# Kernel optimization log

Measured on AMD Instinct MI355X. Metric: run time of the kernel, lower is better.

## Reference

```python
import jax, jax.numpy as jnp
import numpy as np

B, C, H, W = 4, 256, 64, 64
EPS = 1e-6


def setup_inputs() -> dict:
    key = jax.random.key(0)
    ks = jax.random.split(key, 6)
    x = jax.random.normal(ks[0], (B, C, H, W), jnp.float32)
    gn_w = jnp.ones((1, C, 1, 1), jnp.float32)
    gn_b = jnp.zeros((1, C, 1, 1), jnp.float32)
    s = 1.0 / np.sqrt(C)
    w0 = jax.random.normal(ks[1], (C, C), jnp.float32) * s
    w1 = jax.random.normal(ks[2], (C, C), jnp.float32) * s
    w2 = jax.random.normal(ks[3], (C, C), jnp.float32) * s
    w3 = jax.random.normal(ks[4], (C, C), jnp.float32) * s
    b0 = jnp.zeros((C,), jnp.float32)
    b1 = jnp.zeros((C,), jnp.float32)
    b2 = jnp.zeros((C,), jnp.float32)
    b3 = jnp.zeros((C,), jnp.float32)
    return {"x": x, "gn_w": gn_w, "gn_b": gn_b,
            "w0": w0, "b0": b0, "w1": w1, "b1": b1,
            "w2": w2, "b2": b2, "w3": w3, "b3": b3}


def _nin(t, Wm, bv):
    # 1x1 conv as channel matmul: (B,C,H,W) x (C,D) -> (B,D,H,W)
    return jnp.einsum('bchw,cd->bdhw', t, Wm) + bv[None, :, None, None]


def reference(x, gn_w, gn_b, w0, b0, w1, b1, w2, b2, w3, b3):
    Bb, Cc, Hh, Ww = x.shape
    G = min(Cc // 4, 32)  # GroupLayerNorm2d groups
    # per-pixel group norm: normalize over channels within each group only
    xg = x.reshape(Bb, G, Cc // G, Hh, Ww)
    mean = xg.mean(axis=2, keepdims=True)
    var = xg.var(axis=2, keepdims=True)
    hn = ((xg - mean) / jnp.sqrt(var + EPS)).reshape(Bb, Cc, Hh, Ww)
    hn = hn * gn_w + gn_b
    q = _nin(hn, w0, b0)
    k = _nin(hn, w1, b1)
    v = _nin(hn, w2, b2)
    # full (B,H,W,H,W) scores; mask is causal along W only (key col j > query col w)
    scores = jnp.einsum('bchw,bcij->bhwij', q, k) * (float(Cc) ** -0.5)
    causal = jnp.triu(jnp.ones((Ww, Ww), bool), k=1)  # (W_query, W_key)
    scores = jnp.where(causal[None, None, :, None, :], -jnp.inf, scores)
    attn = jax.nn.softmax(scores.reshape(Bb, Hh, Ww, Hh * Ww), axis=-1)
    attn = attn.reshape(Bb, Hh, Ww, Hh, Ww)
    h = jnp.einsum('bhwij,bcij->bchw', attn, v)
    return x + _nin(h, w3, b3)  # skip_rescale=False
```

## Files before the change

### kernel.cpp

```cpp
#include <hip/hip_runtime.h>
#include <math.h>

#define LOG2E 1.4426950408889634f

typedef __attribute__((ext_vector_type(8))) __bf16 bf16x8_t;
typedef __attribute__((ext_vector_type(8))) short short8_t;
typedef __attribute__((ext_vector_type(4))) short short4_t;
typedef __attribute__((ext_vector_type(4))) float f32x4;

static __device__ __forceinline__ short f2bf(float f){
    unsigned u = __builtin_bit_cast(unsigned, f);
    unsigned r = (u + 0x7fffu + ((u >> 16) & 1u)) >> 16;
    return (short)r;
}
static __device__ __forceinline__ float bf2f(short s){
    return __builtin_bit_cast(float, (unsigned)((unsigned short)s) << 16);
}

static __device__ __forceinline__ f32x4 mfma16(short8_t a, short8_t b, f32x4 c){
    return __builtin_amdgcn_mfma_f32_16x16x32_bf16(
        __builtin_bit_cast(bf16x8_t, a), __builtin_bit_cast(bf16x8_t, b), c, 0, 0, 0);
}

static __device__ __forceinline__ float swz16(float v){
    return __builtin_bit_cast(float,
        __builtin_amdgcn_ds_swizzle(__builtin_bit_cast(int, v), 0x401F));
}
static __device__ __forceinline__ float bperm32(int addr, float v){
    return __builtin_bit_cast(float,
        __builtin_amdgcn_ds_bpermute(addr, __builtin_bit_cast(int, v)));
}

__global__ __launch_bounds__(256) void prep_w(const float* __restrict__ w0,
    const float* __restrict__ w1, const float* __restrict__ w2,
    const float* __restrict__ w3, short* __restrict__ wT)
{
    __shared__ float T[64 * 65];
    const int mat = blockIdx.x >> 4, tile = blockIdx.x & 15;
    const int c0 = (tile >> 2) * 64, d0 = (tile & 3) * 64;
    const float* src = mat == 0 ? w0 : mat == 1 ? w1 : mat == 2 ? w2 : w3;
    const int t = threadIdx.x;
    #pragma unroll
    for (int i = 0; i < 4; i++){
        int r = (t >> 4) + i * 16, c4 = (t & 15) * 4;
        f32x4 v = *(const f32x4*)(src + (size_t)(c0 + r) * 256 + d0 + c4);
        #pragma unroll
        for (int j = 0; j < 4; j++) T[r * 65 + c4 + j] = v[j];
    }
    __syncthreads();
    int drow = t >> 2, cb = (t & 3) * 16;
    short tmp[16];
    #pragma unroll
    for (int j = 0; j < 16; j++) tmp[j] = f2bf(T[(cb + j) * 65 + drow]);
    short* dst = wT + (size_t)mat * 65536 + (size_t)(d0 + drow) * 256 + c0 + cb;
    *(short8_t*)dst = *(short8_t*)tmp;
    *(short8_t*)(dst + 8) = *(short8_t*)(tmp + 8);
}

__global__ __launch_bounds__(256) void gn_kernel(const float* __restrict__ x,
    const float* __restrict__ gnw, const float* __restrict__ gnb,
    short* __restrict__ hn)
{
    int flat = blockIdx.x * 256 + threadIdx.x;
    int n = flat & 4095, g = (flat >> 12) & 31, b = flat >> 17;
    const float* xp = x + (size_t)(b * 256 + g * 8) * 4096 + n;
    float v[8], s = 0.f, s2 = 0.f;
    #pragma unroll
    for (int k = 0; k < 8; k++){ float t = xp[(size_t)k * 4096]; v[k] = t; s += t; s2 += t * t; }
    float mean = s * 0.125f;
    float var  = s2 * 0.125f - mean * mean;
    float inv  = rsqrtf(var + 1e-6f);
    int h = n >> 6, w = n & 63, m = w * 64 + h;
    short o[8];
    #pragma unroll
    for (int k = 0; k < 8; k++)
        o[k] = f2bf((v[k] - mean) * inv * gnw[g * 8 + k] + gnb[g * 8 + k]);
    *(short8_t*)(hn + (size_t)(b * 4096 + m) * 256 + g * 8) = *(short8_t*)o;
}

__global__ __launch_bounds__(256) void qkv_gemm(const short* __restrict__ hn,
    const short* __restrict__ wT, const float* __restrict__ bq,
    const float* __restrict__ bk, const float* __restrict__ bv,
    short* __restrict__ Q, short* __restrict__ Kf, short* __restrict__ Vf)
{
    __shared__ short As[64 * 72];
    __shared__ short Bs[64 * 72];
    __shared__ float CT[64 * 65];

    const int tid = threadIdx.x;
    const int m0 = blockIdx.x * 64;
    const int by = blockIdx.y;
    const int mat = by >> 2;
    const int d0 = (by & 3) * 64;
    const short* w = wT + mat * 65536;
    const float* bias = mat == 0 ? bq : mat == 1 ? bk : bv;

    const int wv = tid >> 6, lane = tid & 63;
    const int wrow = (wv >> 1) * 32, wcol = (wv & 1) * 32;
    const int lrow = lane & 15, lq = lane >> 4;

    f32x4 acc[2][2] = {};

    for (int k0 = 0; k0 < 256; k0 += 64){
        __syncthreads();
        #pragma unroll
        for (int i = 0; i < 2; i++){
            int idx = tid + i * 256, r = idx >> 3, c = (idx & 7) * 8;
            *(short8_t*)&As[r * 72 + c] = *(const short8_t*)(hn + (size_t)(m0 + r) * 256 + k0 + c);
            *(short8_t*)&Bs[r * 72 + c] = *(const short8_t*)(w  + (size_t)(d0 + r) * 256 + k0 + c);
        }
        __syncthreads();
        #pragma unroll
        for (int kk = 0; kk < 2; kk++){
            int off = kk * 32 + lq * 8;
            short8_t a0  = *(short8_t*)&As[(wrow + lrow) * 72 + off];
            short8_t a1  = *(short8_t*)&As[(wrow + 16 + lrow) * 72 + off];
            short8_t b0v = *(short8_t*)&Bs[(wcol + lrow) * 72 + off];
            short8_t b1v = *(short8_t*)&Bs[(wcol + 16 + lrow) * 72 + off];
            acc[0][0] = mfma16(a0, b0v, acc[0][0]);
            acc[0][1] = mfma16(a0, b1v, acc[0][1]);
            acc[1][0] = mfma16(a1, b0v, acc[1][0]);
            acc[1][1] = mfma16(a1, b1v, acc[1][1]);
        }
    }

    const int b = m0 >> 12, kb64 = (m0 & 4095) >> 6;

    if (mat == 0){
        #pragma unroll
        for (int i = 0; i < 2; i++)
          #pragma unroll
          for (int j = 0; j < 2; j++)
            #pragma unroll
            for (int r = 0; r < 4; r++){
                int row = wrow + i * 16 + lq * 4 + r;
                int col = wcol + j * 16 + lrow;
                Q[(size_t)(m0 + row) * 256 + d0 + col] = f2bf((acc[i][j][r] + bias[d0 + col]) * 0.0625f);
            }
    } else if (mat == 1){
        #pragma unroll
        for (int i = 0; i < 2; i++)
          #pragma unroll
          for (int j = 0; j < 2; j++)
            #pragma unroll
            for (int r = 0; r < 4; r++){
                int row = wrow + i * 16 + lq * 4 + r;
                int col = wcol + j * 16 + lrow;
                CT[row * 65 + col] = acc[i][j][r] + bias[d0 + col];
            }
        __syncthreads();
        int key = tid >> 2, c16 = (tid & 3) * 16;
        int kc = key >> 4, l15 = key & 15;
        #pragma unroll
        for (int half = 0; half < 2; half++){
            int ch0 = c16 + half * 8;
            int ks = (d0 + ch0) >> 5, lqf = (ch0 & 31) >> 3;
            short tmp[8];
            #pragma unroll
            for (int j = 0; j < 8; j++) tmp[j] = f2bf(CT[key * 65 + ch0 + j]);
            size_t base = ((((size_t)(b * 64 + kb64)) * 4 + kc) * 8 + ks) * 512 + (lqf * 16 + l15) * 8;
            *(short8_t*)(Kf + base) = *(short8_t*)tmp;
        }
    } else {
        #pragma unroll
        for (int i = 0; i < 2; i++)
          #pragma unroll
          for (int j = 0; j < 2; j++)
            #pragma unroll
            for (int r = 0; r < 4; r++){
                int row = wrow + i * 16 + lq * 4 + r;
                int col = wcol + j * 16 + lrow;
                CT[col * 65 + row] = acc[i][j][r] + bias[d0 + col];
            }
        __syncthreads();
        const int kbd = kb64 >> 1, parity = kb64 & 1;
        const int cht_l = tid >> 6, lane_s = tid & 63;
        const int l15s = lane_s & 15, lg4s = lane_s >> 4;
        const int cht = (d0 >> 4) + cht_l;
        #pragma unroll
        for (int kc = 0; kc < 4; kc++){
            short tmp[4];
            #pragma unroll
            for (int j = 0; j < 4; j++)
                tmp[j] = f2bf(CT[(cht_l * 16 + l15s) * 65 + kc * 16 + lg4s * 4 + j]);
            size_t base = (size_t)b * 1048576 + (size_t)kbd * 32768 + kc * 8192
                        + cht * 512 + lane_s * 8 + parity * 4;
            *(short4_t*)(Vf + base) = *(short4_t*)tmp;
        }
    }
}

static __device__ __forceinline__ void sm_update(const f32x4& st, float& m, float& l,
    f32x4* __restrict__ oacc, f32x4* __restrict__ pa, f32x4& p, int a32)
{
    float tmax = fmaxf(fmaxf(st[0], st[1]), fmaxf(st[2], st[3]));
    tmax = fmaxf(tmax, swz16(tmax));
    tmax = fmaxf(tmax, bperm32(a32, tmax));
    if (!__all(tmax <= m + 5.0f)){
        float mn = fmaxf(m, tmax);
        float alpha = exp2f((m - mn) * LOG2E);
        l *= alpha;
        #pragma unroll
        for (int i = 0; i < 16; i++){
            f32x4 t = oacc[i];
            #pragma unroll
            for (int r = 0; r < 4; r++) t[r] *= alpha;
            oacc[i] = t;
        }
        if (pa){
            #pragma unroll
            for (int r = 0; r < 4; r++) (*pa)[r] *= alpha;
        }
        m = mn;
    }
    #pragma unroll
    for (int r = 0; r < 4; r++) p[r] = exp2f((st[r] - m) * LOG2E);
    float ts = (p[0] + p[1]) + (p[2] + p[3]);
    ts += swz16(ts);
    ts += bperm32(a32, ts);
    l += ts;
}

__global__ __launch_bounds__(256, 2) void attn_kernel(const short* __restrict__ Q,
    const short* __restrict__ Kf, const short* __restrict__ Vf,
    short* __restrict__ hb)
{
    __shared__ float mls[4][32][2];
    __shared__ short LOs[4][32][264];

    const int tid = threadIdx.x, lane = tid & 63, kc = tid >> 6;
    const int l15 = lane & 15, lg4 = lane >> 4;
    const int a32 = ((lane ^ 32) << 2);

    const int id  = blockIdx.x;
    const int xcd = id & 7;
    const int b   = xcd >> 1;
    const int hh  = xcd & 1;
    const int r_  = id >> 3;
    const int t_  = r_ & 31;
    const int w   = (r_ >> 5) ? 63 - t_ : t_;
    const int q0  = w * 64 + hh * 32;

    const short* Kb = Kf + (size_t)b * 1048576 + kc * 4096 + lane * 8;
    const short* Vb = Vf + (size_t)b * 1048576 + kc * 8192 + lane * 8;

    short8_t qf0[8], qf1[8];
    {
        const short* qp0 = Q + ((size_t)b * 4096 + q0 + l15) * 256;
        const short* qp1 = qp0 + 16 * 256;
        #pragma unroll
        for (int ks = 0; ks < 8; ks++){
            qf0[ks] = *(const short8_t*)(qp0 + ks * 32 + lg4 * 8);
            qf1[ks] = *(const short8_t*)(qp1 + ks * 32 + lg4 * 8);
        }
    }

    f32x4 oacc0[16] = {}, oacc1[16] = {};
    float m0 = -1e30f, l0 = 0.f;
    float m1 = -1e30f, l1 = 0.f;

    for (int kb = 0; kb <= w; kb += 2){
        short8_t kf[8];
        {
            const short* ka = Kb + (size_t)kb * 16384;
            #pragma unroll
            for (int ks = 0; ks < 8; ks++) kf[ks] = *(const short8_t*)(ka + ks * 512);
        }
        f32x4 stA0 = {}, stA1 = {};
        #pragma unroll
        for (int ks = 0; ks < 8; ks++){
            stA0 = mfma16(kf[ks], qf0[ks], stA0);
            stA1 = mfma16(kf[ks], qf1[ks], stA1);
        }
        f32x4 pa0, pa1;
        sm_update(stA0, m0, l0, oacc0, nullptr, pa0, a32);
        sm_update(stA1, m1, l1, oacc1, nullptr, pa1, a32);

        f32x4 pb0 = {0.f, 0.f, 0.f, 0.f}, pb1 = {0.f, 0.f, 0.f, 0.f};
        if (kb + 1 <= w){
            const short* ka = Kb + (size_t)(kb + 1) * 16384;
            #pragma unroll
            for (int ks = 0; ks < 8; ks++) kf[ks] = *(const short8_t*)(ka + ks * 512);
            f32x4 stB0 = {}, stB1 = {};
            #pragma unroll
            for (int ks = 0; ks < 8; ks++){
                stB0 = mfma16(kf[ks], qf0[ks], stB0);
                stB1 = mfma16(kf[ks], qf1[ks], stB1);
            }
            sm_update(stB0, m0, l0, oacc0, &pa0, pb0, a32);
            sm_update(stB1, m1, l1, oacc1, &pa1, pb1, a32);
        }

        short pk0[8], pk1[8];
        #pragma unroll
        for (int r = 0; r < 4; r++){
            pk0[r] = f2bf(pa0[r]); pk0[4 + r] = f2bf(pb0[r]);
            pk1[r] = f2bf(pa1[r]); pk1[4 + r] = f2bf(pb1[r]);
        }
        short8_t pbf0 = *(short8_t*)pk0;
        short8_t pbf1 = *(short8_t*)pk1;

        const short* vit = Vb + (size_t)(kb >> 1) * 32768;
        #pragma unroll
        for (int cht = 0; cht < 16; cht++){
            short8_t vfr = *(const short8_t*)(vit + cht * 512);
            oacc0[cht] = mfma16(vfr, pbf0, oacc0[cht]);
            oacc1[cht] = mfma16(vfr, pbf1, oacc1[cht]);
        }
    }

    if (lg4 == 0){
        mls[kc][l15][0] = m0;      mls[kc][l15][1] = l0;
        mls[kc][16 + l15][0] = m1; mls[kc][16 + l15][1] = l1;
    }
    __syncthreads();
    float sc0, sc1;
    {
        float ms0 = fmaxf(fmaxf(mls[0][l15][0], mls[1][l15][0]),
                          fmaxf(mls[2][l15][0], mls[3][l15][0]));
        float ms1 = fmaxf(fmaxf(mls[0][16 + l15][0], mls[1][16 + l15][0]),
                          fmaxf(mls[2][16 + l15][0], mls[3][16 + l15][0]));
        sc0 = exp2f((m0 - ms0) * LOG2E);
        sc1 = exp2f((m1 - ms1) * LOG2E);
    }
    #pragma unroll
    for (int cht = 0; cht < 16; cht++){
        short t4[4];
        #pragma unroll
        for (int r = 0; r < 4; r++) t4[r] = f2bf(oacc0[cht][r] * sc0);
        *(short4_t*)&LOs[kc][l15][cht * 16 + lg4 * 4] = *(short4_t*)t4;
        #pragma unroll
        for (int r = 0; r < 4; r++) t4[r] = f2bf(oacc1[cht][r] * sc1);
        *(short4_t*)&LOs[kc][16 + l15][cht * 16 + lg4 * 4] = *(short4_t*)t4;
    }
    __syncthreads();
    {
        const int qq = tid & 31, cc = tid >> 5;
        float mv0 = mls[0][qq][0], mv1 = mls[1][qq][0], mv2 = mls[2][qq][0], mv3 = mls[3][qq][0];
        float ms = fmaxf(fmaxf(mv0, mv1), fmaxf(mv2, mv3));
        float Ls = mls[0][qq][1] * exp2f((mv0 - ms) * LOG2E)
                 + mls[1][qq][1] * exp2f((mv1 - ms) * LOG2E)
                 + mls[2][qq][1] * exp2f((mv2 - ms) * LOG2E)
                 + mls[3][qq][1] * exp2f((mv3 - ms) * LOG2E);
        float inv = 1.f / Ls;
        const int h = hh * 32 + qq;
        short* dst = hb + ((size_t)b * 4096 + h * 64 + w) * 256 + cc * 32;
        #pragma unroll
        for (int c8 = 0; c8 < 4; c8++){
            short8_t a0 = *(const short8_t*)&LOs[0][qq][cc * 32 + c8 * 8];
            short8_t a1 = *(const short8_t*)&LOs[1][qq][cc * 32 + c8 * 8];
            short8_t a2 = *(const short8_t*)&LOs[2][qq][cc * 32 + c8 * 8];
            short8_t a3 = *(const short8_t*)&LOs[3][qq][cc * 32 + c8 * 8];
            short t8[8];
            #pragma unroll
            for (int j = 0; j < 8; j++){
                float s = (bf2f(a0[j]) + bf2f(a1[j])) + (bf2f(a2[j]) + bf2f(a3[j]));
                t8[j] = f2bf(s * inv);
            }
            *(short8_t*)(dst + c8 * 8) = *(short8_t*)t8;
        }
    }
}

__global__ __launch_bounds__(256) void final_gemm(const short* __restrict__ hbuf,
    const short* __restrict__ wT3, const float* __restrict__ b3,
    const float* __restrict__ x, float* __restrict__ out)
{
    __shared__ short As[64 * 72];
    __shared__ short Bs[64 * 72];
    __shared__ float CT[64 * 65];

    const int tid = threadIdx.x;
    const int m0 = blockIdx.x * 64;
    const int d0 = blockIdx.y * 64;
    const int wv = tid >> 6, lane = tid & 63;
    const int wrow = (wv >> 1) * 32, wcol = (wv & 1) * 32;
    const int lrow = lane & 15, lq = lane >> 4;

    f32x4 acc[2][2] = {};
    for (int k0 = 0; k0 < 256; k0 += 64){
        __syncthreads();
        #pragma unroll
        for (int i = 0; i < 2; i++){
            int idx = tid + i * 256, r = idx >> 3, c = (idx & 7) * 8;
            *(short8_t*)&As[r * 72 + c] = *(const short8_t*)(hbuf + (size_t)(m0 + r) * 256 + k0 + c);
            *(short8_t*)&Bs[r * 72 + c] = *(const short8_t*)(wT3 + (size_t)(d0 + r) * 256 + k0 + c);
        }
        __syncthreads();
        #pragma unroll
        for (int kk = 0; kk < 2; kk++){
            int off = kk * 32 + lq * 8;
            short8_t a0  = *(short8_t*)&As[(wrow + lrow) * 72 + off];
            short8_t a1  = *(short8_t*)&As[(wrow + 16 + lrow) * 72 + off];
            short8_t b0v = *(short8_t*)&Bs[(wcol + lrow) * 72 + off];
            short8_t b1v = *(short8_t*)&Bs[(wcol + 16 + lrow) * 72 + off];
            acc[0][0] = mfma16(a0, b0v, acc[0][0]);
            acc[0][1] = mfma16(a0, b1v, acc[0][1]);
            acc[1][0] = mfma16(a1, b0v, acc[1][0]);
            acc[1][1] = mfma16(a1, b1v, acc[1][1]);
        }
    }
    #pragma unroll
    for (int i = 0; i < 2; i++)
      #pragma unroll
      for (int j = 0; j < 2; j++)
        #pragma unroll
        for (int r = 0; r < 4; r++){
            int row = wrow + i * 16 + lq * 4 + r;
            int col = wcol + j * 16 + lrow;
            CT[col * 65 + row] = acc[i][j][r] + b3[d0 + col];
        }
    __syncthreads();
    int b = m0 >> 12, n0 = m0 & 4095, hrow = n0 >> 6;
    int dr = tid >> 2, wc = (tid & 3) * 16;
    size_t base = ((size_t)(b * 256 + d0 + dr) * 64 + hrow) * 64 + wc;
    const f32x4* xp = (const f32x4*)(x + base);
    f32x4* op = (f32x4*)(out + base);
    #pragma unroll
    for (int q = 0; q < 4; q++){
        f32x4 xv = xp[q], o;
        #pragma unroll
        for (int j = 0; j < 4; j++) o[j] = xv[j] + CT[dr * 65 + wc + q * 4 + j];
        op[q] = o;
    }
}

extern "C" void kernel_launch(void* const* d_in, const int* in_sizes, int n_in,
                              void* d_out, int out_size, void* d_ws, size_t ws_size,
                              hipStream_t stream)
{
    const float* x   = (const float*)d_in[0];
    const float* gnw = (const float*)d_in[1];
    const float* gnb = (const float*)d_in[2];
    const float* w0  = (const float*)d_in[3];
    const float* b0  = (const float*)d_in[4];
    const float* w1  = (const float*)d_in[5];
    const float* b1  = (const float*)d_in[6];
    const float* w2  = (const float*)d_in[7];
    const float* b2  = (const float*)d_in[8];
    const float* w3  = (const float*)d_in[9];
    const float* b3  = (const float*)d_in[10];
    float* out = (float*)d_out;

    char* ws = (char*)d_ws;
    short* wT  = (short*)(ws);
    short* hn  = (short*)(ws + 524288);
    short* Qb  = (short*)(ws + 8912896);
    short* Kfb = (short*)(ws + 17301504);
    short* Vfb = (short*)(ws + 25690112);
    short* hb  = (short*)(ws + 34078720);

    prep_w   <<<64, 256, 0, stream>>>(w0, w1, w2, w3, wT);
    gn_kernel<<<2048, 256, 0, stream>>>(x, gnw, gnb, hn);
    qkv_gemm <<<dim3(256, 12), 256, 0, stream>>>(hn, wT, b0, b1, b2, Qb, Kfb, Vfb);
    attn_kernel<<<512, 256, 0, stream>>>(Qb, Kfb, Vfb, hb);
    final_gemm<<<dim3(256, 4), 256, 0, stream>>>(hb, wT + 3 * 65536, b3, x, out);
}
```

Baseline: 244.3 us.

## Prefetch K fragments and stage V via async global-to-LDS loads in attention

```diff
diff --git a/kernel.cpp b/kernel.cpp
--- a/kernel.cpp
+++ b/kernel.cpp
@@ -29,6 +29,12 @@
 static __device__ __forceinline__ float bperm32(int addr, float v){
     return __builtin_bit_cast(float,
         __builtin_amdgcn_ds_bpermute(addr, __builtin_bit_cast(int, v)));
+}
+
+static __device__ __forceinline__ void gload_lds16(const void* g, void* l){
+    __builtin_amdgcn_global_load_lds(
+        (const __attribute__((address_space(1))) unsigned char*)g,
+        (__attribute__((address_space(3))) unsigned char*)l, 16, 0, 0);
 }
 
 __global__ __launch_bounds__(256) void prep_w(const float* __restrict__ w0,
@@ -190,43 +196,12 @@
     }
 }
 
-static __device__ __forceinline__ void sm_update(const f32x4& st, float& m, float& l,
-    f32x4* __restrict__ oacc, f32x4* __restrict__ pa, f32x4& p, int a32)
-{
-    float tmax = fmaxf(fmaxf(st[0], st[1]), fmaxf(st[2], st[3]));
-    tmax = fmaxf(tmax, swz16(tmax));
-    tmax = fmaxf(tmax, bperm32(a32, tmax));
-    if (!__all(tmax <= m + 5.0f)){
-        float mn = fmaxf(m, tmax);
-        float alpha = exp2f((m - mn) * LOG2E);
-        l *= alpha;
-        #pragma unroll
-        for (int i = 0; i < 16; i++){
-            f32x4 t = oacc[i];
-            #pragma unroll
-            for (int r = 0; r < 4; r++) t[r] *= alpha;
-            oacc[i] = t;
-        }
-        if (pa){
-            #pragma unroll
-            for (int r = 0; r < 4; r++) (*pa)[r] *= alpha;
-        }
-        m = mn;
-    }
-    #pragma unroll
-    for (int r = 0; r < 4; r++) p[r] = exp2f((st[r] - m) * LOG2E);
-    float ts = (p[0] + p[1]) + (p[2] + p[3]);
-    ts += swz16(ts);
-    ts += bperm32(a32, ts);
-    l += ts;
-}
-
 __global__ __launch_bounds__(256, 2) void attn_kernel(const short* __restrict__ Q,
     const short* __restrict__ Kf, const short* __restrict__ Vf,
     short* __restrict__ hb)
 {
+    __shared__ short SH[4 * 32 * 264];
     __shared__ float mls[4][32][2];
-    __shared__ short LOs[4][32][264];
 
     const int tid = threadIdx.x, lane = tid & 63, kc = tid >> 6;
     const int l15 = lane & 15, lg4 = lane >> 4;
@@ -238,11 +213,12 @@
     const int hh  = xcd & 1;
     const int r_  = id >> 3;
     const int t_  = r_ & 31;
-    const int w   = (r_ >> 5) ? 63 - t_ : t_;
+    const int w   = (r_ & 32) ? 63 - t_ : t_;
     const int q0  = w * 64 + hh * 32;
 
     const short* Kb = Kf + (size_t)b * 1048576 + kc * 4096 + lane * 8;
-    const short* Vb = Vf + (size_t)b * 1048576 + kc * 8192 + lane * 8;
+    const short* Vg = Vf + (size_t)b * 1048576 + kc * 8192 + lane * 8;
+    short* Vl = &SH[kc * 8192];
 
     short8_t qf0[8], qf1[8];
     {
@@ -259,59 +235,124 @@
     float m0 = -1e30f, l0 = 0.f;
     float m1 = -1e30f, l1 = 0.f;
 
+    short8_t kf[8];
+    #pragma unroll
+    for (int ks = 0; ks < 8; ks++) kf[ks] = *(const short8_t*)(Kb + ks * 512);
+
     for (int kb = 0; kb <= w; kb += 2){
-        short8_t kf[8];
-        {
-            const short* ka = Kb + (size_t)kb * 16384;
-            #pragma unroll
-            for (int ks = 0; ks < 8; ks++) kf[ks] = *(const short8_t*)(ka + ks * 512);
-        }
+        const bool has_odd = (kb + 1 <= w);
+
         f32x4 stA0 = {}, stA1 = {};
         #pragma unroll
         for (int ks = 0; ks < 8; ks++){
             stA0 = mfma16(kf[ks], qf0[ks], stA0);
             stA1 = mfma16(kf[ks], qf1[ks], stA1);
         }
-        f32x4 pa0, pa1;
-        sm_update(stA0, m0, l0, oacc0, nullptr, pa0, a32);
-        sm_update(stA1, m1, l1, oacc1, nullptr, pa1, a32);
-
-        f32x4 pb0 = {0.f, 0.f, 0.f, 0.f}, pb1 = {0.f, 0.f, 0.f, 0.f};
-        if (kb + 1 <= w){
+        if (has_odd){
             const short* ka = Kb + (size_t)(kb + 1) * 16384;
             #pragma unroll
             for (int ks = 0; ks < 8; ks++) kf[ks] = *(const short8_t*)(ka + ks * 512);
+        }
+        {
+            const short* vsrc = Vg + (size_t)(kb >> 1) * 32768;
+            #pragma unroll
+            for (int i = 0; i < 16; i++)
+                gload_lds16(vsrc + i * 512, Vl + i * 512);
+        }
+
+        f32x4 pA0, pA1;
+        {
+            float tl0 = fmaxf(fmaxf(stA0[0], stA0[1]), fmaxf(stA0[2], stA0[3]));
+            float tl1 = fmaxf(fmaxf(stA1[0], stA1[1]), fmaxf(stA1[2], stA1[3]));
+            if (!__all(tl0 <= m0 + 5.f && tl1 <= m1 + 5.f)){
+                float tm0 = fmaxf(tl0, swz16(tl0)); tm0 = fmaxf(tm0, bperm32(a32, tm0));
+                float tm1 = fmaxf(tl1, swz16(tl1)); tm1 = fmaxf(tm1, bperm32(a32, tm1));
+                float mn0 = fmaxf(m0, tm0), mn1 = fmaxf(m1, tm1);
+                float al0 = exp2f((m0 - mn0) * LOG2E), al1 = exp2f((m1 - mn1) * LOG2E);
+                l0 *= al0; l1 *= al1;
+                #pragma unroll
+                for (int i = 0; i < 16; i++){
+                    #pragma unroll
+                    for (int r = 0; r < 4; r++){ oacc0[i][r] *= al0; oacc1[i][r] *= al1; }
+                }
+                m0 = mn0; m1 = mn1;
+            }
+            #pragma unroll
+            for (int r = 0; r < 4; r++){
+                pA0[r] = exp2f((stA0[r] - m0) * LOG2E);
+                pA1[r] = exp2f((stA1[r] - m1) * LOG2E);
+            }
+            l0 += (pA0[0] + pA0[1]) + (pA0[2] + pA0[3]);
+            l1 += (pA1[0] + pA1[1]) + (pA1[2] + pA1[3]);
+        }
+
+        f32x4 pB0 = {0.f, 0.f, 0.f, 0.f}, pB1 = {0.f, 0.f, 0.f, 0.f};
+        if (has_odd){
             f32x4 stB0 = {}, stB1 = {};
             #pragma unroll
             for (int ks = 0; ks < 8; ks++){
                 stB0 = mfma16(kf[ks], qf0[ks], stB0);
                 stB1 = mfma16(kf[ks], qf1[ks], stB1);
             }
-            sm_update(stB0, m0, l0, oacc0, &pa0, pb0, a32);
-            sm_update(stB1, m1, l1, oacc1, &pa1, pb1, a32);
+            if (kb + 2 <= w){
+                const short* ka = Kb + (size_t)(kb + 2) * 16384;
+                #pragma unroll
+                for (int ks = 0; ks < 8; ks++) kf[ks] = *(const short8_t*)(ka + ks * 512);
+            }
+            float tl0 = fmaxf(fmaxf(stB0[0], stB0[1]), fmaxf(stB0[2], stB0[3]));
+            float tl1 = fmaxf(fmaxf(stB1[0], stB1[1]), fmaxf(stB1[2], stB1[3]));
+            if (!__all(tl0 <= m0 + 5.f && tl1 <= m1 + 5.f)){
+                float tm0 = fmaxf(tl0, swz16(tl0)); tm0 = fmaxf(tm0, bperm32(a32, tm0));
+                float tm1 = fmaxf(tl1, swz16(tl1)); tm1 = fmaxf(tm1, bperm32(a32, tm1));
+                float mn0 = fmaxf(m0, tm0), mn1 = fmaxf(m1, tm1);
+                float al0 = exp2f((m0 - mn0) * LOG2E), al1 = exp2f((m1 - mn1) * LOG2E);
+                l0 *= al0; l1 *= al1;
+                #pragma unroll
+                for (int i = 0; i < 16; i++){
+                    #pragma unroll
+                    for (int r = 0; r < 4; r++){ oacc0[i][r] *= al0; oacc1[i][r] *= al1; }
+                }
+                #pragma unroll
+                for (int r = 0; r < 4; r++){ pA0[r] *= al0; pA1[r] *= al1; }
+                m0 = mn0; m1 = mn1;
+            }
+            #pragma unroll
+            for (int r = 0; r < 4; r++){
+                pB0[r] = exp2f((stB0[r] - m0) * LOG2E);
+                pB1[r] = exp2f((stB1[r] - m1) * LOG2E);
+            }
+            l0 += (pB0[0] + pB0[1]) + (pB0[2] + pB0[3]);
+            l1 += (pB1[0] + pB1[1]) + (pB1[2] + pB1[3]);
         }
 
         short pk0[8], pk1[8];
         #pragma unroll
         for (int r = 0; r < 4; r++){
-            pk0[r] = f2bf(pa0[r]); pk0[4 + r] = f2bf(pb0[r]);
-            pk1[r] = f2bf(pa1[r]); pk1[4 + r] = f2bf(pb1[r]);
+            pk0[r] = f2bf(pA0[r]); pk0[4 + r] = f2bf(pB0[r]);
+            pk1[r] = f2bf(pA1[r]); pk1[4 + r] = f2bf(pB1[r]);
         }
         short8_t pbf0 = *(short8_t*)pk0;
         short8_t pbf1 = *(short8_t*)pk1;
 
-        const short* vit = Vb + (size_t)(kb >> 1) * 32768;
+        if (kb + 2 <= w){
+            asm volatile("s_waitcnt vmcnt(8)" ::: "memory");
+        } else {
+            asm volatile("s_waitcnt vmcnt(0)" ::: "memory");
+        }
         #pragma unroll
         for (int cht = 0; cht < 16; cht++){
-            short8_t vfr = *(const short8_t*)(vit + cht * 512);
+            short8_t vfr = *(const short8_t*)(Vl + cht * 512 + lane * 8);
             oacc0[cht] = mfma16(vfr, pbf0, oacc0[cht]);
             oacc1[cht] = mfma16(vfr, pbf1, oacc1[cht]);
         }
     }
 
+    float l0t = l0 + swz16(l0); l0t += bperm32(a32, l0t);
+    float l1t = l1 + swz16(l1); l1t += bperm32(a32, l1t);
+
     if (lg4 == 0){
-        mls[kc][l15][0] = m0;      mls[kc][l15][1] = l0;
-        mls[kc][16 + l15][0] = m1; mls[kc][16 + l15][1] = l1;
+        mls[kc][l15][0] = m0;      mls[kc][l15][1] = l0t;
+        mls[kc][16 + l15][0] = m1; mls[kc][16 + l15][1] = l1t;
     }
     __syncthreads();
     float sc0, sc1;
@@ -328,10 +369,10 @@
         short t4[4];
         #pragma unroll
         for (int r = 0; r < 4; r++) t4[r] = f2bf(oacc0[cht][r] * sc0);
-        *(short4_t*)&LOs[kc][l15][cht * 16 + lg4 * 4] = *(short4_t*)t4;
+        *(short4_t*)&SH[((kc * 32) + l15) * 264 + cht * 16 + lg4 * 4] = *(short4_t*)t4;
         #pragma unroll
         for (int r = 0; r < 4; r++) t4[r] = f2bf(oacc1[cht][r] * sc1);
-        *(short4_t*)&LOs[kc][16 + l15][cht * 16 + lg4 * 4] = *(short4_t*)t4;
+        *(short4_t*)&SH[((kc * 32) + 16 + l15) * 264 + cht * 16 + lg4 * 4] = *(short4_t*)t4;
     }
     __syncthreads();
     {
@@ -347,10 +388,10 @@
         short* dst = hb + ((size_t)b * 4096 + h * 64 + w) * 256 + cc * 32;
         #pragma unroll
         for (int c8 = 0; c8 < 4; c8++){
-            short8_t a0 = *(const short8_t*)&LOs[0][qq][cc * 32 + c8 * 8];
-            short8_t a1 = *(const short8_t*)&LOs[1][qq][cc * 32 + c8 * 8];
-            short8_t a2 = *(const short8_t*)&LOs[2][qq][cc * 32 + c8 * 8];
-            short8_t a3 = *(const short8_t*)&LOs[3][qq][cc * 32 + c8 * 8];
+            short8_t a0 = *(const short8_t*)&SH[((0 * 32) + qq) * 264 + cc * 32 + c8 * 8];
+            short8_t a1 = *(const short8_t*)&SH[((1 * 32) + qq) * 264 + cc * 32 + c8 * 8];
+            short8_t a2 = *(const short8_t*)&SH[((2 * 32) + qq) * 264 + cc * 32 + c8 * 8];
+            short8_t a3 = *(const short8_t*)&SH[((3 * 32) + qq) * 264 + cc * 32 + c8 * 8];
             short t8[8];
             #pragma unroll
             for (int j = 0; j < 8; j++){
```

Result: faster. 204.0 us (-16.5%).
